# Kernel tuning notes

Measured on AMD Instinct MI355X. Metric: run time of the kernel, lower is better.

The kernel has to match this reference:

```python
import jax, jax.numpy as jnp
import numpy as np

B, S, D = 4, 2048, 1024
H = 16
HD = D // H  # 64


def setup_inputs() -> dict:
    key = jax.random.key(0)
    kx, kq, kp = jax.random.split(key, 3)
    x = jax.random.normal(kx, (B, S, D), dtype=jnp.float32)
    # torch Linear weights are [out, in]; match init scale ~ U(-1/sqrt(in), 1/sqrt(in))
    lim = 1.0 / np.sqrt(D)
    w_qkv = jax.random.uniform(kq, (3 * D, D), dtype=jnp.float32, minval=-lim, maxval=lim)
    w_proj = jax.random.uniform(kp, (D, D), dtype=jnp.float32, minval=-lim, maxval=lim)
    return {"x": x, "w_qkv": w_qkv, "w_proj": w_proj}


def reference(x, w_qkv, w_proj):
    b, s, d = x.shape
    qkv = jnp.einsum('bsd,ed->bse', x, w_qkv)  # [B,S,3D]
    q, k, v = jnp.split(qkv, 3, axis=-1)
    # [B,H,S,HD]
    q = q.reshape(b, s, H, HD).transpose(0, 2, 1, 3)
    k = k.reshape(b, s, H, HD).transpose(0, 2, 1, 3)
    v = v.reshape(b, s, H, HD).transpose(0, 2, 1, 3)
    scale = 1.0 / np.sqrt(HD)
    attn = jnp.einsum('bhqd,bhkd->bhqk', q, k) * scale  # [B,H,S,S]
    causal = jnp.tril(jnp.ones((s, s), dtype=bool))
    attn = jnp.where(causal[None, None], attn, -jnp.inf)
    attn = jax.nn.softmax(attn, axis=-1)
    out = jnp.einsum('bhqk,bhkd->bhqd', attn, v)
    out = out.transpose(0, 2, 1, 3).reshape(b, s, d)
    return jnp.einsum('bsd,ed->bse', out, w_proj)
```

## Files before the change

kernel.cpp:

```cpp
#include <hip/hip_runtime.h>

typedef unsigned short u16;
typedef unsigned int u32;

#define B_ 4
#define S_ 2048
#define D_ 1024
#define H_ 16
#define HD_ 64
#define M_ (B_ * S_)
#define QK_ (2 * D_)
#define NP_ 32
#define LOG2E 1.442695041f

typedef __bf16 bf16x8 __attribute__((ext_vector_type(8)));
typedef float f32x4 __attribute__((ext_vector_type(4)));

#define MASKVAL (-1.0e30f)
#define RESCALE_THR 8.0f

static __device__ __forceinline__ u16 f2bf_hw(float f) {
    union { __bf16 b; u16 u; } v;
    v.b = (__bf16)f;
    return v.u;
}

static __device__ __forceinline__ void gload16(const u16* g, u16* l) {
    __builtin_amdgcn_global_load_lds(
        (const __attribute__((address_space(1))) void*)g,
        (__attribute__((address_space(3))) void*)l, 16, 0, 0);
}

static __device__ __forceinline__ void cvt_body(const float* __restrict__ src,
                                                u16* __restrict__ dst, size_t blk,
                                                int tid) {
    size_t i = (blk * 256 + tid) * 8;
    float4 a = *(const float4*)(src + i);
    float4 b = *(const float4*)(src + i + 4);
    union { u16 h[8]; int4 v; } pk;
    pk.h[0] = f2bf_hw(a.x); pk.h[1] = f2bf_hw(a.y);
    pk.h[2] = f2bf_hw(a.z); pk.h[3] = f2bf_hw(a.w);
    pk.h[4] = f2bf_hw(b.x); pk.h[5] = f2bf_hw(b.y);
    pk.h[6] = f2bf_hw(b.z); pk.h[7] = f2bf_hw(b.w);
    *(int4*)(dst + i) = pk.v;
}

__global__ __launch_bounds__(256) void cvt_xw(const float* __restrict__ x,
                                              const float* __restrict__ wqkv,
                                              u16* __restrict__ xb,
                                              u16* __restrict__ wqkvb) {
    int bid = blockIdx.x;
    if (bid < 4096) cvt_body(x, xb, bid, threadIdx.x);
    else            cvt_body(wqkv, wqkvb, bid - 4096, threadIdx.x);
}

__global__ __launch_bounds__(256) void cvt_one(const float* __restrict__ src,
                                               u16* __restrict__ dst) {
    cvt_body(src, dst, blockIdx.x, threadIdx.x);
}

template <int EPI, int BM, int TPB>
__global__ __launch_bounds__(TPB, (TPB == 512) ? 4 : 2)
void gemm8p(const u16* __restrict__ A, const u16* __restrict__ Bw,
            void* __restrict__ Cout, void* __restrict__ C2,
            int Ndim, int strideA, int strideB) {
    __shared__ u16 As[3][BM * 32];
    __shared__ u16 Bs[3][128 * 32];
    constexpr int LA = (BM * 4) / TPB;
    constexpr int LB = 512 / TPB;
    constexpr int L = LA + LB;
    const int t = threadIdx.x;
    const int wave = t >> 6, lane = t & 63;
    const int ml = lane & 15, quad = lane >> 4;
    const int wr = wave >> 1, wc = wave & 1;
    const int bx = blockIdx.x, by = blockIdx.y;
    const int rowA0 = by * BM, rowB0 = bx * 128;

    f32x4 acc[4][4];
    const f32x4 zero = {0.f, 0.f, 0.f, 0.f};
#pragma unroll
    for (int i = 0; i < 4; ++i)
#pragma unroll
        for (int j = 0; j < 4; ++j) acc[i][j] = zero;

    auto STAGE = [&](int slot, int pnl) {
        const int colbase = pnl * 32;
#pragma unroll
        for (int l = 0; l < LA; ++l) {
            const int base = l * TPB + wave * 64;
            const int idx = base + lane;
            const int row = idx >> 2;
            const int sch = ((idx & 3) ^ ((idx >> 3) & 3)) * 8;
            gload16(&A[(size_t)(rowA0 + row) * strideA + colbase + sch],
                    &As[slot][base * 8]);
        }
#pragma unroll
        for (int l = 0; l < LB; ++l) {
            const int base = l * TPB + wave * 64;
            const int idx = base + lane;
            const int row = idx >> 2;
            const int sch = ((idx & 3) ^ ((idx >> 3) & 3)) * 8;
            gload16(&Bw[(size_t)(rowB0 + row) * strideB + colbase + sch],
                    &Bs[slot][base * 8]);
        }
    };

    STAGE(0, 0);
    STAGE(1, 1);
    if constexpr (L == 3) { asm volatile("s_waitcnt vmcnt(3)" ::: "memory"); }
    else                  { asm volatile("s_waitcnt vmcnt(4)" ::: "memory"); }
    __builtin_amdgcn_s_barrier();

    for (int p = 0; p < NP_; ++p) {
        const int slot = p % 3;
        bf16x8 a[4], b[4];
#pragma unroll
        for (int i = 0; i < 4; ++i) {
            const int row = wr * 64 + i * 16 + ml;
            a[i] = *(const bf16x8*)(&As[slot][row * 32 + ((quad ^ ((row >> 1) & 3)) << 3)]);
        }
#pragma unroll
        for (int j = 0; j < 4; ++j) {
            const int row = wc * 64 + j * 16 + ml;
            b[j] = *(const bf16x8*)(&Bs[slot][row * 32 + ((quad ^ ((row >> 1) & 3)) << 3)]);
        }
        if (p + 2 < NP_) STAGE((p + 2) % 3, p + 2);
        asm volatile("s_waitcnt lgkmcnt(0)" ::: "memory");
        __builtin_amdgcn_sched_barrier(0);
        __builtin_amdgcn_s_setprio(1);
#pragma unroll
        for (int i = 0; i < 4; ++i)
#pragma unroll
            for (int j = 0; j < 4; ++j)
                acc[i][j] = __builtin_amdgcn_mfma_f32_16x16x32_bf16(a[i], b[j], acc[i][j], 0, 0, 0);
        __builtin_amdgcn_s_setprio(0);
        if (p + 2 < NP_) {
            if constexpr (L == 3) { asm volatile("s_waitcnt vmcnt(3)" ::: "memory"); }
            else                  { asm volatile("s_waitcnt vmcnt(4)" ::: "memory"); }
        } else {
            asm volatile("s_waitcnt vmcnt(0)" ::: "memory");
        }
        __builtin_amdgcn_s_barrier();
    }

    if constexpr (EPI == 2) {
        float* C = (float*)Cout;
#pragma unroll
        for (int i = 0; i < 4; ++i)
#pragma unroll
            for (int j = 0; j < 4; ++j)
#pragma unroll
                for (int r = 0; r < 4; ++r) {
                    int row = rowA0 + wr * 64 + i * 16 + quad * 4 + r;
                    int col = rowB0 + wc * 64 + j * 16 + ml;
                    C[(size_t)row * Ndim + col] = acc[i][j][r];
                }
    } else {
        if (bx < 16) {
            u16* C = (u16*)Cout;
#pragma unroll
            for (int i = 0; i < 4; ++i)
#pragma unroll
                for (int j = 0; j < 4; ++j)
#pragma unroll
                    for (int r = 0; r < 4; ++r) {
                        int row = rowA0 + wr * 64 + i * 16 + quad * 4 + r;
                        int col = rowB0 + wc * 64 + j * 16 + ml;
                        C[(size_t)row * Ndim + col] = f2bf_hw(acc[i][j][r]);
                    }
        } else {
            u16* Vt = (u16*)C2;
#pragma unroll
            for (int i = 0; i < 4; ++i)
#pragma unroll
                for (int j = 0; j < 4; ++j) {
                    int row0 = rowA0 + wr * 64 + i * 16 + quad * 4;
                    int col = rowB0 + wc * 64 + j * 16 + ml - 2048;
                    int b = row0 >> 11;
                    int s0 = row0 & (S_ - 1);
                    union { u16 h[4]; ushort4 v; } pk;
#pragma unroll
                    for (int r = 0; r < 4; ++r) pk.h[r] = f2bf_hw(acc[i][j][r]);
                    *(ushort4*)(&Vt[((size_t)(b * D_ + col)) * S_ + s0]) = pk.v;
                }
        }
    }
}

__global__ __launch_bounds__(256, 3) void attn3(u16* __restrict__ qk,
                                                const u16* __restrict__ Vt) {
    __shared__ u16 Klds[2][64 * 64];
    __shared__ u16 Vlds[2][64 * 64];
    __shared__ u16 Pw[4][32 * 72];
    const int t = threadIdx.x;
    const int wave = t >> 6, lane = t & 63;
    const int ml = lane & 15, quad = lane >> 4;
    const int mhx = (ml & 8) >> 1;

    const int jj = blockIdx.x >> 6;
    const int bh = blockIdx.x & 63;
    const int t4 = jj >> 2, r4 = jj & 3;
    const int j = (t4 < 2) ? (15 - 4 * t4 - r4) : (12 - 4 * t4 + r4);
    const int b = bh >> 4, h = bh & 15;
    const size_t rowbase = (size_t)b * S_;

    const int srow8 = lane >> 3;
    const int schunk = ((lane & 7) ^ srow8) * 8;

    const int qj0 = j * 128 + wave * 32;
    const int ktw = 2 * j + (wave >> 1);
    const int ktmax = 2 * j + 1;

    u16* pwb = &Pw[wave][0];

    bf16x8 qf[2][2];
#pragma unroll
    for (int mi = 0; mi < 2; ++mi)
#pragma unroll
        for (int kc = 0; kc < 2; ++kc) {
            bf16x8 q = *(const bf16x8*)(&qk[(rowbase + qj0 + mi * 16 + ml) * QK_ +
                                            h * HD_ + kc * 32 + quad * 8]);
#pragma unroll
            for (int e = 0; e < 8; ++e) {
                float f = (float)q[e] * 0.125f;
                q[e] = (__bf16)f;
            }
            qf[mi][kc] = q;
        }

    f32x4 o[2][4];
    float m[2], ls[2];
    const f32x4 zero = {0.f, 0.f, 0.f, 0.f};
#pragma unroll
    for (int mi = 0; mi < 2; ++mi) {
#pragma unroll
        for (int nd = 0; nd < 4; ++nd) o[mi][nd] = zero;
        m[mi] = MASKVAL; ls[mi] = 0.f;
    }

    bf16x8 vf[4][2];

    auto STAGE = [&](int buf, int kt) {
        const int kb = kt * 64;
#pragma unroll
        for (int p = 0; p < 2; ++p) {
            const int rbase = wave * 16 + p * 8;
            gload16(&qk[(rowbase + kb + rbase + srow8) * QK_ + D_ + h * HD_ + schunk],
                    &Klds[buf][rbase * 64]);
            gload16(&Vt[(size_t)(bh * HD_ + rbase + srow8) * S_ + kb + schunk],
                    &Vlds[buf][rbase * 64]);
        }
    };

    auto PV = [&]() {
        bf16x8 pf[2][2];
#pragma unroll
        for (int mi = 0; mi < 2; ++mi)
#pragma unroll
            for (int kc = 0; kc < 2; ++kc)
                pf[mi][kc] = *(const bf16x8*)(&pwb[(mi * 16 + ml) * 72 +
                                                   (((kc * 4 + quad) ^ mhx) << 3)]);
        __builtin_amdgcn_s_setprio(1);
#pragma unroll
        for (int mi = 0; mi < 2; ++mi)
#pragma unroll
            for (int nd = 0; nd < 4; ++nd)
#pragma unroll
                for (int kc = 0; kc < 2; ++kc)
                    o[mi][nd] = __builtin_amdgcn_mfma_f32_16x16x32_bf16(pf[mi][kc], vf[nd][kc],
                                                                        o[mi][nd], 0, 0, 0);
        __builtin_amdgcn_s_setprio(0);
    };

    STAGE(0, 0);

    for (int kt = 0; kt <= ktmax; ++kt) {
        const int cur = kt & 1;
        if (kt < ktmax) STAGE(cur ^ 1, kt + 1);

        if (kt >= 1 && kt - 1 <= ktw) PV();

        if (kt < ktmax) {
            asm volatile("s_waitcnt vmcnt(4)" ::: "memory");
        } else {
            asm volatile("s_waitcnt vmcnt(0)" ::: "memory");
        }
        __builtin_amdgcn_s_barrier();

        if (kt <= ktw) {
            const int kb = kt * 64;
            f32x4 sc[2][4];
            __builtin_amdgcn_s_setprio(1);
#pragma unroll
            for (int ni = 0; ni < 4; ++ni) {
                const int row = ni * 16 + ml;
                bf16x8 kfa = *(const bf16x8*)(&Klds[cur][row * 64 + ((quad ^ (ml & 7)) << 3)]);
                bf16x8 kfb = *(const bf16x8*)(&Klds[cur][row * 64 + (((4 + quad) ^ (ml & 7)) << 3)]);
#pragma unroll
                for (int mi = 0; mi < 2; ++mi) {
                    f32x4 s = __builtin_amdgcn_mfma_f32_16x16x32_bf16(kfa, qf[mi][0], zero, 0, 0, 0);
                    sc[mi][ni] = __builtin_amdgcn_mfma_f32_16x16x32_bf16(kfb, qf[mi][1], s, 0, 0, 0);
                }
            }
            __builtin_amdgcn_s_setprio(0);

            if (kb + 63 > qj0) {
#pragma unroll
                for (int mi = 0; mi < 2; ++mi) {
                    const int q = qj0 + mi * 16 + ml;
#pragma unroll
                    for (int ni = 0; ni < 4; ++ni)
#pragma unroll
                        for (int r = 0; r < 4; ++r) {
                            int k = kb + ni * 16 + quad * 4 + r;
                            if (k > q) sc[mi][ni][r] = MASKVAL;
                        }
                }
            }

#pragma unroll
            for (int mi = 0; mi < 2; ++mi) {
                float tm = sc[mi][0][0];
#pragma unroll
                for (int ni = 0; ni < 4; ++ni)
#pragma unroll
                    for (int r = 0; r < 4; ++r) tm = fmaxf(tm, sc[mi][ni][r]);
                tm = fmaxf(tm, __shfl_xor(tm, 16, 64));
                tm = fmaxf(tm, __shfl_xor(tm, 32, 64));
                if (__any(tm > m[mi] + RESCALE_THR)) {
                    float mn = fmaxf(m[mi], tm);
                    float al = __builtin_amdgcn_exp2f((m[mi] - mn) * LOG2E);
                    m[mi] = mn;
                    ls[mi] *= al;
                    float alr[4];
#pragma unroll
                    for (int r = 0; r < 4; ++r)
                        alr[r] = __shfl(al, (lane & 48) + ((lane & 48) >> 2) + r, 64);
#pragma unroll
                    for (int nd = 0; nd < 4; ++nd)
#pragma unroll
                        for (int r = 0; r < 4; ++r) o[mi][nd][r] *= alr[r];
                }
                const float mm = m[mi] * LOG2E;
                float sum = 0.f;
#pragma unroll
                for (int ni = 0; ni < 4; ++ni)
#pragma unroll
                    for (int r = 0; r < 4; ++r) {
                        float e = __builtin_amdgcn_exp2f(__builtin_fmaf(sc[mi][ni][r], LOG2E, -mm));
                        sc[mi][ni][r] = e;
                        sum += e;
                    }
                ls[mi] += sum;
#pragma unroll
                for (int ni = 0; ni < 4; ++ni) {
                    union { u16 h[4]; ushort4 v; } pk;
#pragma unroll
                    for (int r = 0; r < 4; ++r) pk.h[r] = f2bf_hw(sc[mi][ni][r]);
                    const int off = (mi * 16 + ml) * 72 +
                                    ((((2 * ni + (quad >> 1)) ^ mhx)) << 3) + ((quad & 1) << 2);
                    *(ushort4*)(&pwb[off]) = pk.v;
                }
            }
#pragma unroll
            for (int ni = 0; ni < 4; ++ni) {
                const int row = ni * 16 + ml;
#pragma unroll
                for (int kc = 0; kc < 2; ++kc)
                    vf[ni][kc] = *(const bf16x8*)(&Vlds[cur][row * 64 +
                                                            (((kc * 4 + quad) ^ (ml & 7)) << 3)]);
            }
        }
        asm volatile("s_waitcnt lgkmcnt(0)" ::: "memory");
        __builtin_amdgcn_s_barrier();
    }

    if (ktw == ktmax) PV();

#pragma unroll
    for (int mi = 0; mi < 2; ++mi) {
        float s = ls[mi];
        s += __shfl_xor(s, 16, 64);
        s += __shfl_xor(s, 32, 64);
        float rl = 1.0f / s;
        float rlr[4];
#pragma unroll
        for (int r = 0; r < 4; ++r)
            rlr[r] = __shfl(rl, (lane & 48) + ((lane & 48) >> 2) + r, 64);
#pragma unroll
        for (int nd = 0; nd < 4; ++nd)
#pragma unroll
            for (int r = 0; r < 4; ++r) {
                int srow = qj0 + mi * 16 + quad * 4 + r;
                qk[(rowbase + srow) * QK_ + h * HD_ + nd * 16 + ml] =
                    f2bf_hw(o[mi][nd][r] * rlr[r]);
            }
    }
}

extern "C" void kernel_launch(void* const* d_in, const int* in_sizes, int n_in,
                              void* d_out, int out_size, void* d_ws, size_t ws_size,
                              hipStream_t stream) {
    const float* x = (const float*)d_in[0];
    const float* wqkv = (const float*)d_in[1];
    const float* wproj = (const float*)d_in[2];
    float* out = (float*)d_out;

    u16* qkw = (u16*)d_ws;
    u16* Vtw = qkw + (size_t)M_ * QK_;

    u16* xb = (u16*)d_out;
    u16* wqkvb = xb + (size_t)M_ * D_;

    cvt_xw<<<dim3(4096 + 1536), 256, 0, stream>>>(x, wqkv, xb, wqkvb);

    gemm8p<3, 256, 512><<<dim3(3 * D_ / 128, M_ / 256), 512, 0, stream>>>(
        xb, wqkvb, qkw, Vtw, QK_, D_, D_);

    attn3<<<dim3(1024), 256, 0, stream>>>(qkw, Vtw);

    cvt_one<<<dim3(512), 256, 0, stream>>>(wproj, Vtw);

    gemm8p<2, 128, 256><<<dim3(D_ / 128, M_ / 128), 256, 0, stream>>>(
        qkw, Vtw, out, nullptr, D_, QK_, D_);
}
```

Measured before the change: 244.3 us.

## Add 256x256-tile QKV GEMM kernel with split-B MFMA scheduling

Replaces the 256x128 tile QKV projection GEMM with a dedicated 256x256 tile kernel using 8 waves in a 2x4 layout, each computing 128x64 of output. The larger tile halves the number of blocks and raises arithmetic intensity per LDS load. B fragment loads are split into two halves so MFMAs on the first half can overlap the LDS reads of the second, with setprio hints around the MFMA bursts. The cost is more LDS (96KB) and more accumulator registers, which may limit occupancy, and only 12x32=384 blocks are launched.

```diff
diff --git a/kernel.cpp b/kernel.cpp
--- a/kernel.cpp
+++ b/kernel.cpp
@@ -57,6 +57,125 @@
 __global__ __launch_bounds__(256) void cvt_one(const float* __restrict__ src,
                                                u16* __restrict__ dst) {
     cvt_body(src, dst, blockIdx.x, threadIdx.x);
+}
+
+__global__ __launch_bounds__(512, 2)
+void gemm256(const u16* __restrict__ A, const u16* __restrict__ Bw,
+             u16* __restrict__ Cqk, u16* __restrict__ Vt) {
+    __shared__ u16 As[3][256 * 32];
+    __shared__ u16 Bs[3][256 * 32];
+    const int t = threadIdx.x;
+    const int wave = t >> 6, lane = t & 63;
+    const int ml = lane & 15, quad = lane >> 4;
+    const int wr = wave >> 2, wc = wave & 3;
+    const int bx = blockIdx.x, by = blockIdx.y;
+    const int rowA0 = by * 256, rowB0 = bx * 256;
+
+    f32x4 acc[8][4];
+    const f32x4 zero = {0.f, 0.f, 0.f, 0.f};
+#pragma unroll
+    for (int i = 0; i < 8; ++i)
+#pragma unroll
+        for (int j = 0; j < 4; ++j) acc[i][j] = zero;
+
+    auto STAGE = [&](int slot, int pnl) {
+        const int colbase = pnl * 32;
+#pragma unroll
+        for (int l = 0; l < 2; ++l) {
+            const int base = l * 512 + wave * 64;
+            const int idx = base + lane;
+            const int row = idx >> 2;
+            const int sch = ((idx & 3) ^ ((idx >> 3) & 3)) * 8;
+            gload16(&A[(size_t)(rowA0 + row) * 1024 + colbase + sch],
+                    &As[slot][base * 8]);
+        }
+#pragma unroll
+        for (int l = 0; l < 2; ++l) {
+            const int base = l * 512 + wave * 64;
+            const int idx = base + lane;
+            const int row = idx >> 2;
+            const int sch = ((idx & 3) ^ ((idx >> 3) & 3)) * 8;
+            gload16(&Bw[(size_t)(rowB0 + row) * 1024 + colbase + sch],
+                    &Bs[slot][base * 8]);
+        }
+    };
+
+    STAGE(0, 0);
+    STAGE(1, 1);
+    asm volatile("s_waitcnt vmcnt(4)" ::: "memory");
+    __builtin_amdgcn_s_barrier();
+
+    for (int p = 0; p < NP_; ++p) {
+        const int slot = p % 3;
+        bf16x8 a[8], b[4];
+#pragma unroll
+        for (int i = 0; i < 8; ++i) {
+            const int row = wr * 128 + i * 16 + ml;
+            a[i] = *(const bf16x8*)(&As[slot][row * 32 + ((quad ^ ((row >> 1) & 3)) << 3)]);
+        }
+#pragma unroll
+        for (int j = 0; j < 2; ++j) {
+            const int row = wc * 64 + j * 16 + ml;
+            b[j] = *(const bf16x8*)(&Bs[slot][row * 32 + ((quad ^ ((row >> 1) & 3)) << 3)]);
+        }
+        __builtin_amdgcn_sched_barrier(0);
+#pragma unroll
+        for (int j = 2; j < 4; ++j) {
+            const int row = wc * 64 + j * 16 + ml;
+            b[j] = *(const bf16x8*)(&Bs[slot][row * 32 + ((quad ^ ((row >> 1) & 3)) << 3)]);
+        }
+        __builtin_amdgcn_sched_barrier(0);
+        if (p + 2 < NP_) STAGE((p + 2) % 3, p + 2);
+        asm volatile("s_waitcnt lgkmcnt(2)" ::: "memory");
+        __builtin_amdgcn_sched_barrier(0);
+        __builtin_amdgcn_s_setprio(1);
+#pragma unroll
+        for (int i = 0; i < 8; ++i)
+#pragma unroll
+            for (int j = 0; j < 2; ++j)
+                acc[i][j] = __builtin_amdgcn_mfma_f32_16x16x32_bf16(a[i], b[j], acc[i][j], 0, 0, 0);
+        __builtin_amdgcn_s_setprio(0);
+        asm volatile("s_waitcnt lgkmcnt(0)" ::: "memory");
+        __builtin_amdgcn_sched_barrier(0);
+        __builtin_amdgcn_s_setprio(1);
+#pragma unroll
+        for (int i = 0; i < 8; ++i)
+#pragma unroll
+            for (int j = 2; j < 4; ++j)
+                acc[i][j] = __builtin_amdgcn_mfma_f32_16x16x32_bf16(a[i], b[j], acc[i][j], 0, 0, 0);
+        __builtin_amdgcn_s_setprio(0);
+        if (p + 2 < NP_) { asm volatile("s_waitcnt vmcnt(4)" ::: "memory"); }
+        else             { asm volatile("s_waitcnt vmcnt(0)" ::: "memory"); }
+        __builtin_amdgcn_s_barrier();
+    }
+
+    if (bx < 8) {
+        u16* C = Cqk;
+#pragma unroll
+        for (int i = 0; i < 8; ++i)
+#pragma unroll
+            for (int j = 0; j < 4; ++j)
+#pragma unroll
+                for (int r = 0; r < 4; ++r) {
+                    int row = rowA0 + wr * 128 + i * 16 + quad * 4 + r;
+                    int col = rowB0 + wc * 64 + j * 16 + ml;
+                    C[(size_t)row * QK_ + col] = f2bf_hw(acc[i][j][r]);
+                }
+    } else {
+#pragma unroll
+        for (int i = 0; i < 8; ++i)
+#pragma unroll
+            for (int j = 0; j < 4; ++j) {
+                int row0 = rowA0 + wr * 128 + i * 16 + quad * 4;
+                int col = rowB0 + wc * 64 + j * 16 + ml - 2048;
+                int b = row0 >> 11;
+                int s0 = row0 & (S_ - 1);
+                union { u16 h[4]; ushort4 v; } pk;
+#pragma unroll
+                for (int r = 0; r < 4; ++r) pk.h[r] = f2bf_hw(acc[i][j][r]);
+                *(ushort4*)(&Vt[((size_t)(b * D_ + col)) * S_ + s0]) = pk.v;
+            }
+    }
 }
 
 template <int EPI, int BM, int TPB>
@@ -156,34 +275,17 @@
                     C[(size_t)row * Ndim + col] = acc[i][j][r];
                 }
     } else {
-        if (bx < 16) {
-            u16* C = (u16*)Cout;
-#pragma unroll
-            for (int i = 0; i < 4; ++i)
-#pragma unroll
-                for (int j = 0; j < 4; ++j)
-#pragma unroll
-                    for (int r = 0; r < 4; ++r) {
-                        int row = rowA0 + wr * 64 + i * 16 + quad * 4 + r;
-                        int col = rowB0 + wc * 64 + j * 16 + ml;
-                        C[(size_t)row * Ndim + col] = f2bf_hw(acc[i][j][r]);
-                    }
-        } else {
-            u16* Vt = (u16*)C2;
-#pragma unroll
-            for (int i = 0; i < 4; ++i)
-#pragma unroll
-                for (int j = 0; j < 4; ++j) {
-                    int row0 = rowA0 + wr * 64 + i * 16 + quad * 4;
-                    int col = rowB0 + wc * 64 + j * 16 + ml - 2048;
-                    int b = row0 >> 11;
-                    int s0 = row0 & (S_ - 1);
-                    union { u16 h[4]; ushort4 v; } pk;
-#pragma unroll
-                    for (int r = 0; r < 4; ++r) pk.h[r] = f2bf_hw(acc[i][j][r]);
-                    *(ushort4*)(&Vt[((size_t)(b * D_ + col)) * S_ + s0]) = pk.v;
-                }
-        }
+        u16* C = (u16*)Cout;
+#pragma unroll
+        for (int i = 0; i < 4; ++i)
+#pragma unroll
+            for (int j = 0; j < 4; ++j)
+#pragma unroll
+                for (int r = 0; r < 4; ++r) {
+                    int row = rowA0 + wr * 64 + i * 16 + quad * 4 + r;
+                    int col = rowB0 + wc * 64 + j * 16 + ml;
+                    C[(size_t)row * Ndim + col] = f2bf_hw(acc[i][j][r]);
+                }
     }
 }
 
@@ -414,8 +516,8 @@
 
     cvt_xw<<<dim3(4096 + 1536), 256, 0, stream>>>(x, wqkv, xb, wqkvb);
 
-    gemm8p<3, 256, 512><<<dim3(3 * D_ / 128, M_ / 256), 512, 0, stream>>>(
-        xb, wqkvb, qkw, Vtw, QK_, D_, D_);
+    gemm256<<<dim3(3 * D_ / 256, M_ / 256), 512, 0, stream>>>(
+        xb, wqkvb, qkw, Vtw);
 
     attn3<<<dim3(1024), 256, 0, stream>>>(qkw, Vtw);
 
```

After: 243.7 us. About the same (-0.3%).
